# Optimization experiments

Measured on AMD Instinct MI355X. Metric: run time of the kernel, lower is better.

Reference implementation:

```python
import jax, jax.numpy as jnp
import numpy as np

N, T, F = 128, 512, 3
H = 5          # hidden_channels
NEURONS = 2000


def setup_inputs() -> dict:
    key = jax.random.key(0)
    ks = jax.random.split(key, 8)
    s = 0.3  # keep exp() outputs in a sane range
    return {
        "x": jax.random.normal(ks[0], (N, T, F), dtype=jnp.float32),
        "w_ih": jax.random.normal(ks[1], (3 * H, F), dtype=jnp.float32) * s,
        "w_hh": jax.random.normal(ks[2], (3 * H, H), dtype=jnp.float32) * s,
        "b_ih": jax.random.normal(ks[3], (3 * H,), dtype=jnp.float32) * s,
        "b_hh": jax.random.normal(ks[4], (3 * H,), dtype=jnp.float32) * s,
        "lw": jax.random.normal(ks[5], (NEURONS, H), dtype=jnp.float32) * s,
        "lb": jax.random.normal(ks[6], (NEURONS,), dtype=jnp.float32) * s,
    }


def _gru_states(x, w_ih, w_hh, b_ih, b_hh):
    # x: [N, T, F] -> hidden states [T, N, H] via lax.scan (PyTorch GRUCell math)
    n_batch = x.shape[0]
    h0 = jnp.zeros((n_batch, w_hh.shape[1]), dtype=x.dtype)

    def step(h, xt):
        gi = xt @ w_ih.T + b_ih              # [N, 3H]
        gh = h @ w_hh.T + b_hh               # [N, 3H]
        i_r, i_z, i_n = jnp.split(gi, 3, axis=1)
        h_r, h_z, h_n = jnp.split(gh, 3, axis=1)
        r = jax.nn.sigmoid(i_r + h_r)
        z = jax.nn.sigmoid(i_z + h_z)
        n = jnp.tanh(i_n + r * h_n)
        h_new = (1.0 - z) * n + z * h
        return h_new, h_new

    _, hs = jax.lax.scan(step, h0, jnp.swapaxes(x, 0, 1))
    return hs  # [T, N, H]


def reference(x, w_ih, w_hh, b_ih, b_hh, lw, lb):
    hs = _gru_states(x, w_ih, w_hh, b_ih, b_hh)          # [T, N, H]
    states = jnp.swapaxes(hs, 0, 1)                      # [N, T, H] (== stack(states, 1))
    out = jnp.exp(jnp.einsum("nth,oh->nto", states, lw) + lb)  # [N, T, NEURONS]
    return out
```

## Files before the change

kernel.cpp:

```cpp
#include <hip/hip_runtime.h>
#include <hip/hip_bf16.h>

#define N_BATCH 128
#define T_STEPS 512
#define F_IN 3
#define H_DIM 5
#define NEURONS 2000
#define NT (N_BATCH * T_STEPS)
#define SROW 8
#define XLDS_STRIDE 1540

__device__ __forceinline__ float fast_rcp(float x) {
    return __builtin_amdgcn_rcpf(x);
}

__device__ __forceinline__ float fast_sigmoid(float x) {
    return fast_rcp(1.0f + __expf(-x));
}

__device__ __forceinline__ float fast_tanh(float x) {
    float t = __expf(x + x);
    return (t - 1.0f) * fast_rcp(t + 1.0f);
}

__global__ __launch_bounds__(64, 1) void gru_kernel(
    const float* __restrict__ x,
    const float* __restrict__ w_ih,
    const float* __restrict__ w_hh,
    const float* __restrict__ b_ih,
    const float* __restrict__ b_hh,
    float* __restrict__ states)
{
    __shared__ float xs[8 * XLDS_STRIDE];

    const int tid = threadIdx.x;
    const int b   = blockIdx.x;

    const float* xg = x + (size_t)b * 8 * T_STEPS * F_IN;
    for (int e4 = tid; e4 < (8 * T_STEPS * F_IN) / 4; e4 += 64) {
        float4 v = ((const float4*)xg)[e4];
        int e   = e4 * 4;
        int nl  = e / (T_STEPS * F_IN);
        int off = e - nl * (T_STEPS * F_IN);
        float* d = &xs[nl * XLDS_STRIDE + off];
        d[0] = v.x; d[1] = v.y; d[2] = v.z; d[3] = v.w;
    }
    __syncthreads();

    const int nl = tid >> 3;
    const int j  = tid & 7;
    const int jj = (j < 5) ? j : 4;

    float wir[F_IN], wiz[F_IN], win[F_IN];
    float whr[H_DIM], whz[H_DIM], whn[H_DIM];
#pragma unroll
    for (int f = 0; f < F_IN; ++f) {
        wir[f] = w_ih[(jj)            * F_IN + f];
        wiz[f] = w_ih[(H_DIM + jj)    * F_IN + f];
        win[f] = w_ih[(2*H_DIM + jj)  * F_IN + f];
    }
#pragma unroll
    for (int i = 0; i < H_DIM; ++i) {
        whr[i] = w_hh[(jj)            * H_DIM + i];
        whz[i] = w_hh[(H_DIM + jj)    * H_DIM + i];
        whn[i] = w_hh[(2*H_DIM + jj)  * H_DIM + i];
    }
    const float br  = b_ih[jj]          + b_hh[jj];
    const float bz  = b_ih[H_DIM + jj]  + b_hh[H_DIM + jj];
    const float bin = b_ih[2*H_DIM + jj];
    const float bhn = b_hh[2*H_DIM + jj];

    const float* xl = &xs[nl * XLDS_STRIDE];
    float* sp = states + (size_t)(b * 8 + nl) * T_STEPS * SROW;

    float h = 0.0f;
    float nx0 = xl[0], nx1 = xl[1], nx2 = xl[2];

    for (int t = 0; t < T_STEPS; ++t) {
        const float x0 = nx0, x1 = nx1, x2 = nx2;
        nx0 = xl[(t + 1) * 3 + 0];
        nx1 = xl[(t + 1) * 3 + 1];
        nx2 = xl[(t + 1) * 3 + 2];

        const float h0 = __shfl(h, 0, 8);
        const float h1 = __shfl(h, 1, 8);
        const float h2 = __shfl(h, 2, 8);
        const float h3 = __shfl(h, 3, 8);
        const float h4 = __shfl(h, 4, 8);

        float ar = br + x0*wir[0] + x1*wir[1] + x2*wir[2]
                      + h0*whr[0] + h1*whr[1] + h2*whr[2] + h3*whr[3] + h4*whr[4];
        float az = bz + x0*wiz[0] + x1*wiz[1] + x2*wiz[2]
                      + h0*whz[0] + h1*whz[1] + h2*whz[2] + h3*whz[3] + h4*whz[4];
        float gin = bin + x0*win[0] + x1*win[1] + x2*win[2];
        float ghn = bhn + h0*whn[0] + h1*whn[1] + h2*whn[2] + h3*whn[3] + h4*whn[4];

        const float r  = fast_sigmoid(ar);
        const float z  = fast_sigmoid(az);
        const float nn = fast_tanh(gin + r * ghn);
        h = (1.0f - z) * nn + z * h;

        sp[t * SROW + j] = h;
    }
}

__global__ __launch_bounds__(256) void readout_kernel(
    const float* __restrict__ states,
    const float* __restrict__ lw,
    const float* __restrict__ lb,
    float* __restrict__ out)
{
    const int tid = threadIdx.x;
    const int o1 = tid * 4;
    const int o2 = 1024 + tid * 4;
    const bool act2 = o2 < NEURONS;

    float w1[4][H_DIM], b1[4];
    float w2[4][H_DIM], b2[4];
#pragma unroll
    for (int i = 0; i < 4; ++i) {
        b1[i] = lb[o1 + i];
#pragma unroll
        for (int k = 0; k < H_DIM; ++k) w1[i][k] = lw[(o1 + i) * H_DIM + k];
    }
    if (act2) {
#pragma unroll
        for (int i = 0; i < 4; ++i) {
            b2[i] = lb[o2 + i];
#pragma unroll
            for (int k = 0; k < H_DIM; ++k) w2[i][k] = lw[(o2 + i) * H_DIM + k];
        }
    }

    for (int p = blockIdx.x; p < NT; p += gridDim.x) {
        const float* hp = states + (size_t)p * SROW;
        const float4 hv = *(const float4*)hp;
        const float h4  = hp[4];

        float* row = out + (size_t)p * NEURONS;

        float4 v1;
        v1.x = __expf(b1[0] + w1[0][0]*hv.x + w1[0][1]*hv.y + w1[0][2]*hv.z + w1[0][3]*hv.w + w1[0][4]*h4);
        v1.y = __expf(b1[1] + w1[1][0]*hv.x + w1[1][1]*hv.y + w1[1][2]*hv.z + w1[1][3]*hv.w + w1[1][4]*h4);
        v1.z = __expf(b1[2] + w1[2][0]*hv.x + w1[2][1]*hv.y + w1[2][2]*hv.z + w1[2][3]*hv.w + w1[2][4]*h4);
        v1.w = __expf(b1[3] + w1[3][0]*hv.x + w1[3][1]*hv.y + w1[3][2]*hv.z + w1[3][3]*hv.w + w1[3][4]*h4);
        ((float4*)row)[tid] = v1;

        if (act2) {
            float4 v2;
            v2.x = __expf(b2[0] + w2[0][0]*hv.x + w2[0][1]*hv.y + w2[0][2]*hv.z + w2[0][3]*hv.w + w2[0][4]*h4);
            v2.y = __expf(b2[1] + w2[1][0]*hv.x + w2[1][1]*hv.y + w2[1][2]*hv.z + w2[1][3]*hv.w + w2[1][4]*h4);
            v2.z = __expf(b2[2] + w2[2][0]*hv.x + w2[2][1]*hv.y + w2[2][2]*hv.z + w2[2][3]*hv.w + w2[2][4]*h4);
            v2.w = __expf(b2[3] + w2[3][0]*hv.x + w2[3][1]*hv.y + w2[3][2]*hv.z + w2[3][3]*hv.w + w2[3][4]*h4);
            *(float4*)(row + o2) = v2;
        }
    }
}

extern "C" void kernel_launch(void* const* d_in, const int* in_sizes, int n_in,
                              void* d_out, int out_size, void* d_ws, size_t ws_size,
                              hipStream_t stream) {
    const float* x    = (const float*)d_in[0];
    const float* w_ih = (const float*)d_in[1];
    const float* w_hh = (const float*)d_in[2];
    const float* b_ih = (const float*)d_in[3];
    const float* b_hh = (const float*)d_in[4];
    const float* lw   = (const float*)d_in[5];
    const float* lb   = (const float*)d_in[6];
    float* out = (float*)d_out;

    float* states = (float*)d_ws;

    gru_kernel<<<16, 64, 0, stream>>>(x, w_ih, w_hh, b_ih, b_hh, states);
    readout_kernel<<<2048, 256, 0, stream>>>(states, lw, lb, out);
}
```

Measured before the change: 634.9 us.

## Remap GRU recurrence to four lanes per sequence with DPP broadcasts

```diff
diff --git a/kernel.cpp b/kernel.cpp
--- a/kernel.cpp
+++ b/kernel.cpp
@@ -8,19 +8,24 @@
 #define NEURONS 2000
 #define NT (N_BATCH * T_STEPS)
 #define SROW 8
-#define XLDS_STRIDE 1540
+#define C_STEPS 8
+#define N_CHUNKS (T_STEPS / C_STEPS)
+
+#define LOG2E  1.44269504088896340736f
+#define LOG2E2 2.88539008177792681472f
 
 __device__ __forceinline__ float fast_rcp(float x) {
     return __builtin_amdgcn_rcpf(x);
 }
 
-__device__ __forceinline__ float fast_sigmoid(float x) {
-    return fast_rcp(1.0f + __expf(-x));
-}
-
-__device__ __forceinline__ float fast_tanh(float x) {
-    float t = __expf(x + x);
-    return (t - 1.0f) * fast_rcp(t + 1.0f);
+__device__ __forceinline__ float exp2f_hw(float x) {
+    return __builtin_amdgcn_exp2f(x);
+}
+
+template <int LANE>
+__device__ __forceinline__ float quad_bcast(float v) {
+    int i = __builtin_amdgcn_mov_dpp(__float_as_int(v), LANE * 0x55, 0xF, 0xF, false);
+    return __int_as_float(i);
 }
 
 __global__ __launch_bounds__(64, 1) void gru_kernel(
@@ -31,77 +36,125 @@
     const float* __restrict__ b_hh,
     float* __restrict__ states)
 {
-    __shared__ float xs[8 * XLDS_STRIDE];
-
     const int tid = threadIdx.x;
-    const int b   = blockIdx.x;
-
-    const float* xg = x + (size_t)b * 8 * T_STEPS * F_IN;
-    for (int e4 = tid; e4 < (8 * T_STEPS * F_IN) / 4; e4 += 64) {
-        float4 v = ((const float4*)xg)[e4];
-        int e   = e4 * 4;
-        int nl  = e / (T_STEPS * F_IN);
-        int off = e - nl * (T_STEPS * F_IN);
-        float* d = &xs[nl * XLDS_STRIDE + off];
-        d[0] = v.x; d[1] = v.y; d[2] = v.z; d[3] = v.w;
-    }
-    __syncthreads();
-
-    const int nl = tid >> 3;
-    const int j  = tid & 7;
-    const int jj = (j < 5) ? j : 4;
-
-    float wir[F_IN], wiz[F_IN], win[F_IN];
-    float whr[H_DIM], whz[H_DIM], whn[H_DIM];
+    const int gid = blockIdx.x * 64 + tid;
+    const int n   = gid >> 2;
+    const int k   = tid & 3;
+
+    float wirA[F_IN], wizA[F_IN], winA[F_IN], whrA[H_DIM], whzA[H_DIM], whnA[H_DIM];
+    float wirB[F_IN], wizB[F_IN], winB[F_IN], whrB[H_DIM], whzB[H_DIM], whnB[H_DIM];
 #pragma unroll
     for (int f = 0; f < F_IN; ++f) {
-        wir[f] = w_ih[(jj)            * F_IN + f];
-        wiz[f] = w_ih[(H_DIM + jj)    * F_IN + f];
-        win[f] = w_ih[(2*H_DIM + jj)  * F_IN + f];
+        wirA[f] = w_ih[(k)            * F_IN + f] * LOG2E;
+        wizA[f] = w_ih[(H_DIM + k)    * F_IN + f] * LOG2E;
+        winA[f] = w_ih[(2*H_DIM + k)  * F_IN + f] * LOG2E2;
+        wirB[f] = w_ih[(4)            * F_IN + f] * LOG2E;
+        wizB[f] = w_ih[(H_DIM + 4)    * F_IN + f] * LOG2E;
+        winB[f] = w_ih[(2*H_DIM + 4)  * F_IN + f] * LOG2E2;
     }
 #pragma unroll
     for (int i = 0; i < H_DIM; ++i) {
-        whr[i] = w_hh[(jj)            * H_DIM + i];
-        whz[i] = w_hh[(H_DIM + jj)    * H_DIM + i];
-        whn[i] = w_hh[(2*H_DIM + jj)  * H_DIM + i];
-    }
-    const float br  = b_ih[jj]          + b_hh[jj];
-    const float bz  = b_ih[H_DIM + jj]  + b_hh[H_DIM + jj];
-    const float bin = b_ih[2*H_DIM + jj];
-    const float bhn = b_hh[2*H_DIM + jj];
-
-    const float* xl = &xs[nl * XLDS_STRIDE];
-    float* sp = states + (size_t)(b * 8 + nl) * T_STEPS * SROW;
-
-    float h = 0.0f;
-    float nx0 = xl[0], nx1 = xl[1], nx2 = xl[2];
-
-    for (int t = 0; t < T_STEPS; ++t) {
-        const float x0 = nx0, x1 = nx1, x2 = nx2;
-        nx0 = xl[(t + 1) * 3 + 0];
-        nx1 = xl[(t + 1) * 3 + 1];
-        nx2 = xl[(t + 1) * 3 + 2];
-
-        const float h0 = __shfl(h, 0, 8);
-        const float h1 = __shfl(h, 1, 8);
-        const float h2 = __shfl(h, 2, 8);
-        const float h3 = __shfl(h, 3, 8);
-        const float h4 = __shfl(h, 4, 8);
-
-        float ar = br + x0*wir[0] + x1*wir[1] + x2*wir[2]
-                      + h0*whr[0] + h1*whr[1] + h2*whr[2] + h3*whr[3] + h4*whr[4];
-        float az = bz + x0*wiz[0] + x1*wiz[1] + x2*wiz[2]
-                      + h0*whz[0] + h1*whz[1] + h2*whz[2] + h3*whz[3] + h4*whz[4];
-        float gin = bin + x0*win[0] + x1*win[1] + x2*win[2];
-        float ghn = bhn + h0*whn[0] + h1*whn[1] + h2*whn[2] + h3*whn[3] + h4*whn[4];
-
-        const float r  = fast_sigmoid(ar);
-        const float z  = fast_sigmoid(az);
-        const float nn = fast_tanh(gin + r * ghn);
-        h = (1.0f - z) * nn + z * h;
-
-        sp[t * SROW + j] = h;
-    }
+        whrA[i] = w_hh[(k)            * H_DIM + i] * LOG2E;
+        whzA[i] = w_hh[(H_DIM + k)    * H_DIM + i] * LOG2E;
+        whnA[i] = w_hh[(2*H_DIM + k)  * H_DIM + i] * LOG2E2;
+        whrB[i] = w_hh[(4)            * H_DIM + i] * LOG2E;
+        whzB[i] = w_hh[(H_DIM + 4)    * H_DIM + i] * LOG2E;
+        whnB[i] = w_hh[(2*H_DIM + 4)  * H_DIM + i] * LOG2E2;
+    }
+    const float brA  = (b_ih[k]           + b_hh[k])           * LOG2E;
+    const float bzA  = (b_ih[H_DIM + k]   + b_hh[H_DIM + k])   * LOG2E;
+    const float binA =  b_ih[2*H_DIM + k]                      * LOG2E2;
+    const float bhnA =  b_hh[2*H_DIM + k]                      * LOG2E2;
+    const float brB  = (b_ih[4]           + b_hh[4])           * LOG2E;
+    const float bzB  = (b_ih[H_DIM + 4]   + b_hh[H_DIM + 4])   * LOG2E;
+    const float binB =  b_ih[2*H_DIM + 4]                      * LOG2E2;
+    const float bhnB =  b_hh[2*H_DIM + 4]                      * LOG2E2;
+
+    const float* xp = x + (size_t)n * (T_STEPS * F_IN);
+    float* sp = states + (size_t)n * T_STEPS * SROW;
+
+    float hA = 0.0f;
+    float hB = 0.0f;
+
+    float xa[3 * C_STEPS], xb[3 * C_STEPS];
+
+#define LOAD_CHUNK(dst, cc)                                            \
+    {                                                                  \
+        const float4* src = (const float4*)xp + 6 * (cc);              \
+        _Pragma("unroll")                                              \
+        for (int i = 0; i < 6; ++i) {                                  \
+            float4 v = src[i];                                         \
+            dst[4*i+0] = v.x; dst[4*i+1] = v.y;                        \
+            dst[4*i+2] = v.z; dst[4*i+3] = v.w;                        \
+        }                                                              \
+    }
+
+#define STEP(xc, t, so)                                                          \
+    {                                                                            \
+        const float x0 = xc[3*(t)+0], x1 = xc[3*(t)+1], x2 = xc[3*(t)+2];        \
+        const float h0 = quad_bcast<0>(hA);                                      \
+        const float h1 = quad_bcast<1>(hA);                                      \
+        const float h2 = quad_bcast<2>(hA);                                      \
+        const float h3 = quad_bcast<3>(hA);                                      \
+        const float h4 = hB;                                                     \
+        float arA = fmaf(x0,wirA[0], fmaf(x1,wirA[1], fmaf(x2,wirA[2], brA)));   \
+        arA = fmaf(h0,whrA[0], fmaf(h1,whrA[1], fmaf(h2,whrA[2],                 \
+              fmaf(h3,whrA[3], fmaf(h4,whrA[4], arA)))));                        \
+        float azA = fmaf(x0,wizA[0], fmaf(x1,wizA[1], fmaf(x2,wizA[2], bzA)));   \
+        azA = fmaf(h0,whzA[0], fmaf(h1,whzA[1], fmaf(h2,whzA[2],                 \
+              fmaf(h3,whzA[3], fmaf(h4,whzA[4], azA)))));                        \
+        float giA = fmaf(x0,winA[0], fmaf(x1,winA[1], fmaf(x2,winA[2], binA)));  \
+        float ghA = fmaf(h0,whnA[0], fmaf(h1,whnA[1], fmaf(h2,whnA[2],           \
+              fmaf(h3,whnA[3], fmaf(h4,whnA[4], bhnA)))));                       \
+        float arB = fmaf(x0,wirB[0], fmaf(x1,wirB[1], fmaf(x2,wirB[2], brB)));   \
+        arB = fmaf(h0,whrB[0], fmaf(h1,whrB[1], fmaf(h2,whrB[2],                 \
+              fmaf(h3,whrB[3], fmaf(h4,whrB[4], arB)))));                        \
+        float azB = fmaf(x0,wizB[0], fmaf(x1,wizB[1], fmaf(x2,wizB[2], bzB)));   \
+        azB = fmaf(h0,whzB[0], fmaf(h1,whzB[1], fmaf(h2,whzB[2],                 \
+              fmaf(h3,whzB[3], fmaf(h4,whzB[4], azB)))));                        \
+        float giB = fmaf(x0,winB[0], fmaf(x1,winB[1], fmaf(x2,winB[2], binB)));  \
+        float ghB = fmaf(h0,whnB[0], fmaf(h1,whnB[1], fmaf(h2,whnB[2],           \
+              fmaf(h3,whnB[3], fmaf(h4,whnB[4], bhnB)))));                       \
+        const float rA = fast_rcp(1.0f + exp2f_hw(-arA));                        \
+        const float zA = fast_rcp(1.0f + exp2f_hw(-azA));                        \
+        const float tA = exp2f_hw(fmaf(rA, ghA, giA));                           \
+        const float nA = (tA - 1.0f) * fast_rcp(tA + 1.0f);                      \
+        hA = fmaf(zA, hA - nA, nA);                                              \
+        const float rB = fast_rcp(1.0f + exp2f_hw(-arB));                        \
+        const float zB = fast_rcp(1.0f + exp2f_hw(-azB));                        \
+        const float tB = exp2f_hw(fmaf(rB, ghB, giB));                           \
+        const float nB = (tB - 1.0f) * fast_rcp(tB + 1.0f);                      \
+        hB = fmaf(zB, hB - nB, nB);                                              \
+        (so)[(t) * SROW + k] = hA;                                               \
+        if (k == 0) (so)[(t) * SROW + 4] = hB;                                   \
+    }
+
+#define PROC8(xc, so)                                                            \
+    {                                                                            \
+        STEP(xc, 0, so) STEP(xc, 1, so) STEP(xc, 2, so) STEP(xc, 3, so)          \
+        STEP(xc, 4, so) STEP(xc, 5, so) STEP(xc, 6, so) STEP(xc, 7, so)          \
+    }
+
+    LOAD_CHUNK(xa, 0)
+    LOAD_CHUNK(xb, 1)
+
+    for (int c = 0; c < N_CHUNKS; c += 2) {
+        float* soA = sp + (size_t)c * C_STEPS * SROW;
+        PROC8(xa, soA)
+        {
+            int cc = c + 2; if (cc > N_CHUNKS - 2) cc = N_CHUNKS - 2;
+            LOAD_CHUNK(xa, cc)
+        }
+        float* soB = sp + (size_t)(c + 1) * C_STEPS * SROW;
+        PROC8(xb, soB)
+        {
+            int cc = c + 3; if (cc > N_CHUNKS - 1) cc = N_CHUNKS - 1;
+            LOAD_CHUNK(xb, cc)
+        }
+    }
+#undef STEP
+#undef PROC8
+#undef LOAD_CHUNK
 }
 
 __global__ __launch_bounds__(256) void readout_kernel(
@@ -121,14 +174,14 @@
     for (int i = 0; i < 4; ++i) {
         b1[i] = lb[o1 + i];
 #pragma unroll
-        for (int k = 0; k < H_DIM; ++k) w1[i][k] = lw[(o1 + i) * H_DIM + k];
+        for (int kk = 0; kk < H_DIM; ++kk) w1[i][kk] = lw[(o1 + i) * H_DIM + kk];
     }
     if (act2) {
 #pragma unroll
         for (int i = 0; i < 4; ++i) {
             b2[i] = lb[o2 + i];
 #pragma unroll
-            for (int k = 0; k < H_DIM; ++k) w2[i][k] = lw[(o2 + i) * H_DIM + k];
+            for (int kk = 0; kk < H_DIM; ++kk) w2[i][kk] = lw[(o2 + i) * H_DIM + kk];
         }
     }
 
@@ -171,6 +224,6 @@
 
     float* states = (float*)d_ws;
 
-    gru_kernel<<<16, 64, 0, stream>>>(x, w_ih, w_hh, b_ih, b_hh, states);
+    gru_kernel<<<8, 64, 0, stream>>>(x, w_ih, w_hh, b_ih, b_hh, states);
     readout_kernel<<<2048, 256, 0, stream>>>(states, lw, lb, out);
 }
```

New measurement: 629.9 us. About the same (-0.8%).
